# Performance work log

Measured on AMD Instinct MI355X. Metric: run time of the kernel, lower is better.

The kernel has to match this reference:

```python
import jax, jax.numpy as jnp
import numpy as np

K = 16
D_MODEL = 128

def _gather(pts, idx):
    # pts: [B,N,C], idx: [B,N,K] -> [B,N,K,C]
    return jax.vmap(lambda p, i: p[i])(pts, idx)

def setup_inputs() -> dict:
    key = jax.random.key(0)
    ks = jax.random.split(key, 20)
    s = 0.05
    def w(k_, shape):
        return jax.random.normal(k_, shape, dtype=jnp.float32) * s
    B, N, C = 4, 4096, 3
    TF, D = 128, D_MODEL
    return {
        "xyz": jax.random.normal(ks[0], (B, N, C), dtype=jnp.float32),
        "W0a": w(ks[1], (C, TF)),  "b0a": jnp.zeros((TF,), jnp.float32),
        "W0b": w(ks[2], (TF, TF)), "b0b": jnp.zeros((TF,), jnp.float32),
        "W1":  w(ks[3], (TF, D)),  "b1":  jnp.zeros((D,), jnp.float32),
        "W2":  w(ks[4], (D, TF)),  "b2":  jnp.zeros((TF,), jnp.float32),
        "Wd1": w(ks[5], (C, D)),   "bd1": jnp.zeros((D,), jnp.float32),
        "Wd2": w(ks[6], (D, D)),   "bd2": jnp.zeros((D,), jnp.float32),
        "Wg1": w(ks[7], (D, D)),   "bg1": jnp.zeros((D,), jnp.float32),
        "Wg2": w(ks[8], (D, D)),   "bg2": jnp.zeros((D,), jnp.float32),
        "Wq":  w(ks[9], (D, D)),
        "Wk":  w(ks[10], (D, D)),
        "Wv":  w(ks[11], (D, D)),
    }

def reference(xyz, W0a, b0a, W0b, b0b, W1, b1, W2, b2,
              Wd1, bd1, Wd2, bd2, Wg1, bg1, Wg2, bg2, Wq, Wk, Wv):
    sq = jnp.sum(xyz * xyz, axis=-1)
    dists = sq[:, :, None] - 2.0 * jnp.einsum('bnc,bmc->bnm', xyz, xyz) + sq[:, None, :]
    _, knn_idx = jax.lax.top_k(-dists, K)          # [B,N,K] nearest neighbors

    knn_xyz = _gather(xyz, knn_idx)                # [B,N,K,3]
    features = jax.nn.relu(xyz @ W0a + b0a) @ W0b + b0b   # fc0  [B,N,TF]
    pre = features
    x = features @ W1 + b1                          # fc1  [B,N,D]
    q = x @ Wq                                      # [B,N,D]
    kf = _gather(x @ Wk, knn_idx)                   # [B,N,K,D]
    vf = _gather(x @ Wv, knn_idx)                   # [B,N,K,D]

    delta = xyz[:, :, None, :] - knn_xyz            # [B,N,K,3]
    pos_enc = jax.nn.relu(delta @ Wd1 + bd1) @ Wd2 + bd2   # fc_delta [B,N,K,D]

    h = q[:, :, None, :] - kf + pos_enc
    attn_logits = jax.nn.relu(h @ Wg1 + bg1) @ Wg2 + bg2   # fc_gamma [B,N,K,D]
    attn = jax.nn.softmax(attn_logits / np.sqrt(D_MODEL).astype(np.float32), axis=-2)

    res = jnp.einsum('bmnf,bmnf->bmf', attn, vf + pos_enc)  # [B,N,D]
    res = res @ W2 + b2 + pre                               # [B,N,TF]
    return res, attn
```

## Files before the change

### kernel.cpp

```cpp
#include <hip/hip_runtime.h>
#include <math.h>

#define BB 4
#define NN 4096
#define KNNK 16
#define DD 128
#define BN (BB*NN)

typedef __attribute__((ext_vector_type(8))) short short8;
typedef __attribute__((ext_vector_type(4))) float floatx4;

__device__ __forceinline__ short f2bf(float x) {
  __bf16 b = (__bf16)x;
  return (short)__builtin_bit_cast(unsigned short, b);
}

__device__ __forceinline__ float bf2f(short h) {
  return __uint_as_float((unsigned)(unsigned short)h << 16);
}

#define LDSFENCE() asm volatile("s_waitcnt lgkmcnt(0)" ::: "memory")

__device__ __forceinline__ void split_from_lds(const float* __restrict__ trans,
                                               int c, int g, short8 ah[4],
                                               short8 al[4]) {
#pragma unroll
  for (int s = 0; s < 4; ++s) {
    const float* p_ = &trans[c * 132 + s * 32 + g * 8];
    float4 u0 = *reinterpret_cast<const float4*>(p_);
    float4 u1 = *reinterpret_cast<const float4*>(p_ + 4);
    float tmp[8] = {u0.x, u0.y, u0.z, u0.w, u1.x, u1.y, u1.z, u1.w};
#pragma unroll
    for (int j = 0; j < 8; ++j) {
      short h_ = f2bf(tmp[j]);
      ah[s][j] = h_;
      al[s][j] = f2bf(tmp[j] - bf2f(h_));
    }
  }
}

__device__ __forceinline__ void split_gemm2(const short* __restrict__ Bh,
                                            int nt0, int lane,
                                            const short8 ah[4],
                                            const short8 al[4], floatx4& acc0,
                                            floatx4& acc1) {
  const short* Bl = Bh + 16384;
#pragma unroll
  for (int ks = 0; ks < 4; ++ks) {
    const size_t o0 = ((size_t)((nt0 + 0) * 4 + ks) * 64 + lane) * 8;
    const size_t o1 = ((size_t)((nt0 + 1) * 4 + ks) * 64 + lane) * 8;
    short8 bh0 = *reinterpret_cast<const short8*>(Bh + o0);
    short8 bl0 = *reinterpret_cast<const short8*>(Bl + o0);
    short8 bh1 = *reinterpret_cast<const short8*>(Bh + o1);
    short8 bl1 = *reinterpret_cast<const short8*>(Bl + o1);
    acc0 = __builtin_amdgcn_mfma_f32_16x16x32_bf16(ah[ks], bh0, acc0, 0, 0, 0);
    acc1 = __builtin_amdgcn_mfma_f32_16x16x32_bf16(ah[ks], bh1, acc1, 0, 0, 0);
    acc0 = __builtin_amdgcn_mfma_f32_16x16x32_bf16(ah[ks], bl0, acc0, 0, 0, 0);
    acc1 = __builtin_amdgcn_mfma_f32_16x16x32_bf16(ah[ks], bl1, acc1, 0, 0, 0);
    acc0 = __builtin_amdgcn_mfma_f32_16x16x32_bf16(al[ks], bh0, acc0, 0, 0, 0);
    acc1 = __builtin_amdgcn_mfma_f32_16x16x32_bf16(al[ks], bh1, acc1, 0, 0, 0);
  }
}

__device__ __forceinline__ void ced(double& a, double& b) {
  double mn = fmin(a, b);
  double mx = fmax(a, b);
  a = mn;
  b = mx;
}

__device__ __forceinline__ void dsort16(double v[16]) {
#define CE(i, j) ced(v[i], v[j]);
  CE(0, 1) CE(2, 3) CE(4, 5) CE(6, 7) CE(8, 9) CE(10, 11) CE(12, 13) CE(14, 15)
  CE(0, 2) CE(1, 3) CE(4, 6) CE(5, 7) CE(8, 10) CE(9, 11) CE(12, 14) CE(13, 15)
  CE(1, 2) CE(5, 6) CE(9, 10) CE(13, 14)
  CE(0, 4) CE(1, 5) CE(2, 6) CE(3, 7) CE(8, 12) CE(9, 13) CE(10, 14) CE(11, 15)
  CE(2, 4) CE(3, 5) CE(10, 12) CE(11, 13)
  CE(1, 2) CE(3, 4) CE(5, 6) CE(9, 10) CE(11, 12) CE(13, 14)
  CE(0, 8) CE(1, 9) CE(2, 10) CE(3, 11) CE(4, 12) CE(5, 13) CE(6, 14) CE(7, 15)
  CE(4, 8) CE(5, 9) CE(6, 10) CE(7, 11)
  CE(2, 4) CE(3, 5) CE(6, 8) CE(7, 9) CE(10, 12) CE(11, 13)
  CE(1, 2) CE(3, 4) CE(5, 6) CE(7, 8) CE(9, 10) CE(11, 12) CE(13, 14)
#undef CE
}

__device__ __forceinline__ void dbitonic16(double m[16]) {
#pragma unroll
  for (int s = 8; s >= 1; s >>= 1) {
#pragma unroll
    for (int i = 0; i < 16; ++i) {
      if ((i & s) == 0) ced(m[i], m[i + s]);
    }
  }
}

__global__ __launch_bounds__(256, 4) void knn_kernel(
    const float4* __restrict__ pts4, int* __restrict__ knn) {
  const int wv = threadIdx.x >> 6;
  const int lane = threadIdx.x & 63;
  const int ln = lane & 15;
  const int qg = lane >> 4;
  const int q = blockIdx.x * 16 + wv * 4 + qg;
  const int b = q >> 12;
  const int n = q & 4095;
  const float4* pb = pts4 + ((size_t)b << 12);

  const float4 qp = pb[n];
  const float qx = qp.x, qy = qp.y, qz = qp.z, qsq = qp.w;

#define LOADBATCH(batch)                                                       \
  _Pragma("unroll") for (int i = 0; i < 16; ++i) {                             \
    const int c = ((batch) * 16 + i) * 16 + ln;                                \
    float4 p = pb[c];                                                          \
    float dot = __fadd_rn(__fadd_rn(__fmul_rn(qx, p.x), __fmul_rn(qy, p.y)),   \
                          __fmul_rn(qz, p.z));                                 \
    float d = __fadd_rn(__fsub_rn(qsq, __fmul_rn(2.0f, dot)), p.w);            \
    unsigned u = __float_as_uint(d);                                           \
    u = (u & 0x80000000u) ? ~u : (u | 0x80000000u);                            \
    unsigned long long key =                                                   \
        0x3FF0000000000000ULL | (((unsigned long long)u << 12) | (unsigned)c); \
    v[i] = __longlong_as_double((long long)key);                               \
  }

  double top[16];
  {
    double v[16];
    LOADBATCH(0);
    dsort16(v);
#pragma unroll
    for (int i = 0; i < 16; ++i) top[i] = v[i];
  }
#pragma unroll 1
  for (int batch = 1; batch < 16; ++batch) {
    double v[16];
    LOADBATCH(batch);
    dsort16(v);
    double m[16];
#pragma unroll
    for (int i = 0; i < 16; ++i)
      m[i] = fmin(top[i], v[15 - i]);
    dbitonic16(m);
#pragma unroll
    for (int i = 0; i < 16; ++i) top[i] = m[i];
  }
#undef LOADBATCH

#pragma unroll
  for (int mask = 1; mask <= 8; mask <<= 1) {
    double oth[16];
#pragma unroll
    for (int i = 0; i < 16; ++i) {
      double y = __shfl_xor(top[15 - i], mask);
      oth[i] = fmin(y, top[i]);
    }
    dbitonic16(oth);
#pragma unroll
    for (int i = 0; i < 16; ++i) top[i] = oth[i];
  }

  if (ln == 0) {
    int* outp = knn + (size_t)q * KNNK;
#pragma unroll
    for (int k = 0; k < 16; ++k)
      outp[k] = (int)(__double_as_longlong(top[k]) & 0xFFFLL);
  }
}

__global__ void swz_all_kernel(const float* __restrict__ xyz,
                               const float* __restrict__ Wd2,
                               const float* __restrict__ Wg1,
                               const float* __restrict__ Wg2,
                               const float* __restrict__ W0b,
                               const float* __restrict__ W1,
                               const float* __restrict__ Wq,
                               const float* __restrict__ Wk,
                               const float* __restrict__ Wv,
                               const float* __restrict__ W2,
                               short* __restrict__ wsw,
                               short* __restrict__ wsplit,
                               float4* __restrict__ pts4) {
  int t = blockIdx.x * 256 + threadIdx.x;
  if (t < BN) {
    float cx = xyz[(size_t)t * 3 + 0];
    float cy = xyz[(size_t)t * 3 + 1];
    float cz = xyz[(size_t)t * 3 + 2];
    float csq = __fadd_rn(__fadd_rn(__fmul_rn(cx, cx), __fmul_rn(cy, cy)),
                          __fmul_rn(cz, cz));
    pts4[t] = make_float4(cx, cy, cz, csq);
  }
  if (t < 3 * 2048) {
    int stage = t / 2048;
    int rem = t % 2048;
    int nt = rem / 256;
    int ks = (rem % 256) / 64;
    int lane = rem % 64;
    const float* W = (stage == 0) ? Wd2 : (stage == 1) ? Wg1 : Wg2;
    short8 o;
#pragma unroll
    for (int j = 0; j < 8; ++j) {
      int k = ks * 32 + (lane >> 4) * 8 + j;
      int n = nt * 16 + (lane & 15);
      o[j] = f2bf(W[k * 128 + n]);
    }
    *reinterpret_cast<short8*>(wsw + (size_t)t * 8) = o;
  } else {
    int u = t - 3 * 2048;
    if (u >= 6 * 2048) return;
    int mat = u / 2048;
    int rem = u % 2048;
    int nt = rem / 256;
    int ks = (rem % 256) / 64;
    int lane = rem % 64;
    const float* W = (mat == 0) ? W0b : (mat == 1) ? W1 : (mat == 2) ? Wq
                     : (mat == 3) ? Wk : (mat == 4) ? Wv : W2;
    short8 hi, lo;
#pragma unroll
    for (int j = 0; j < 8; ++j) {
      int k = ks * 32 + (lane >> 4) * 8 + j;
      int n = nt * 16 + (lane & 15);
      float w = W[k * 128 + n];
      short h = f2bf(w);
      hi[j] = h;
      lo[j] = f2bf(w - bf2f(h));
    }
    *reinterpret_cast<short8*>(wsplit + ((size_t)(2 * mat) * 2048 + rem) * 8) = hi;
    *reinterpret_cast<short8*>(wsplit + ((size_t)(2 * mat + 1) * 2048 + rem) * 8) = lo;
  }
}

__global__ __launch_bounds__(256, 4) void point_mlp_mfma_kernel(
    const float* __restrict__ xyz, const float* __restrict__ W0a,
    const float* __restrict__ b0a, const float* __restrict__ b0b,
    const float* __restrict__ b1, const short* __restrict__ wsplit,
    float* __restrict__ pre, float* __restrict__ qv, float* __restrict__ kv,
    float* __restrict__ vv) {
  const int wv = threadIdx.x >> 6;
  const int lane = threadIdx.x & 63;
  const int g = lane >> 4;
  const int c = lane & 15;
  const int g0 = blockIdx.x * 16;
  const int nt0 = wv * 2;

  __shared__ __attribute__((aligned(16))) float trans[16 * 132];
  __shared__ float xs[64];
  if (threadIdx.x < 48) {
    int p = threadIdx.x / 3, cc = threadIdx.x % 3;
    xs[p * 4 + cc] = xyz[(size_t)(g0 + p) * 3 + cc];
  }
  __syncthreads();

  short8 ah[4], al[4];
  {
    const float x0 = xs[c * 4 + 0], x1 = xs[c * 4 + 1], x2 = xs[c * 4 + 2];
#pragma unroll
    for (int s = 0; s < 4; ++s) {
#pragma unroll
      for (int j = 0; j < 8; ++j) {
        const int k = s * 32 + g * 8 + j;
        float v = fmaf(x2, W0a[256 + k],
                       fmaf(x1, W0a[128 + k], fmaf(x0, W0a[k], b0a[k])));
        v = fmaxf(v, 0.f);
        const short h = f2bf(v);
        ah[s][j] = h;
        al[s][j] = f2bf(v - bf2f(h));
      }
    }
  }

  floatx4 acc0, acc1;
  const floatx4 zf = (floatx4){0.f, 0.f, 0.f, 0.f};

  acc0 = zf; acc1 = zf;
  split_gemm2(wsplit + 0 * 32768, nt0, lane, ah, al, acc0, acc1);
  {
    const float bb0 = b0b[nt0 * 16 + c];
    const float bb1 = b0b[(nt0 + 1) * 16 + c];
#pragma unroll
    for (int r = 0; r < 4; ++r) {
      const int row = g * 4 + r;
      float v0 = acc0[r] + bb0;
      float v1 = acc1[r] + bb1;
      pre[(size_t)(g0 + row) * 128 + nt0 * 16 + c] = v0;
      pre[(size_t)(g0 + row) * 128 + (nt0 + 1) * 16 + c] = v1;
      trans[row * 132 + nt0 * 16 + c] = v0;
      trans[row * 132 + (nt0 + 1) * 16 + c] = v1;
    }
  }
  __syncthreads();
  split_from_lds(trans, c, g, ah, al);
  __syncthreads();

  acc0 = zf; acc1 = zf;
  split_gemm2(wsplit + 1 * 32768, nt0, lane, ah, al, acc0, acc1);
  {
    const float bb0 = b1[nt0 * 16 + c];
    const float bb1 = b1[(nt0 + 1) * 16 + c];
#pragma unroll
    for (int r = 0; r < 4; ++r) {
      const int row = g * 4 + r;
      trans[row * 132 + nt0 * 16 + c] = acc0[r] + bb0;
      trans[row * 132 + (nt0 + 1) * 16 + c] = acc1[r] + bb1;
    }
  }
  __syncthreads();
  split_from_lds(trans, c, g, ah, al);
  __syncthreads();

#define GSTORE(dst)                                                            \
  _Pragma("unroll") for (int r = 0; r < 4; ++r) {                              \
    const int row = g0 + g * 4 + r;                                            \
    dst[(size_t)row * 128 + nt0 * 16 + c] = acc0[r];                           \
    dst[(size_t)row * 128 + (nt0 + 1) * 16 + c] = acc1[r];                     \
  }

  acc0 = zf; acc1 = zf;
  split_gemm2(wsplit + 2 * 32768, nt0, lane, ah, al, acc0, acc1);
  GSTORE(qv);

  acc0 = zf; acc1 = zf;
  split_gemm2(wsplit + 3 * 32768, nt0, lane, ah, al, acc0, acc1);
  GSTORE(kv);

  acc0 = zf; acc1 = zf;
  split_gemm2(wsplit + 4 * 32768, nt0, lane, ah, al, acc0, acc1);
  GSTORE(vv);

#undef GSTORE
}

__device__ __forceinline__ void wstage(const short* __restrict__ wsw_stage,
                                       short* __restrict__ wlds, int wv,
                                       int lane) {
#pragma unroll
  for (int i = 0; i < 8; ++i) {
    short8 w_ = *reinterpret_cast<const short8*>(wsw_stage + wv * 4096 +
                                                 i * 512 + lane * 8);
    *reinterpret_cast<short8*>(&wlds[wv * 4096 + i * 512 + lane * 8]) = w_;
  }
}

__global__ __launch_bounds__(256, 3) void attn_mfma_kernel(
    const float* __restrict__ xyz, const int* __restrict__ knn,
    const float* __restrict__ qv, const float* __restrict__ kv,
    const float* __restrict__ vv, const short* __restrict__ wsw,
    const float* __restrict__ Wd1, const float* __restrict__ bd1,
    const float* __restrict__ bd2, const float* __restrict__ bg1,
    const float* __restrict__ bg2, float* __restrict__ res_ws,
    float* __restrict__ out_attn) {
  const int wv = threadIdx.x >> 6;
  const int lane = threadIdx.x & 63;
  const int g = lane >> 4;
  const int c = lane & 15;
  const int bn = blockIdx.x * 4 + wv;
  const int b = bn >> 12;
  const int base_n = b << 12;

  __shared__ __attribute__((aligned(16))) short wlds[16384];
  __shared__ __attribute__((aligned(16))) short conv[4][16 * 136];

  const int* knnp = knn + (size_t)bn * 16;
  const int idxn = knnp[c];
  int idxr[4];
#pragma unroll
  for (int r = 0; r < 4; ++r) idxr[r] = knnp[g * 4 + r];

  float kvf[8][4];
#pragma unroll
  for (int nt = 0; nt < 8; ++nt)
#pragma unroll
    for (int r = 0; r < 4; ++r)
      kvf[nt][r] = kv[((size_t)(base_n + idxr[r])) * 128 + nt * 16 + c];

  const float ddx = xyz[(size_t)bn * 3 + 0] - xyz[((size_t)(base_n + idxn)) * 3 + 0];
  const float ddy = xyz[(size_t)bn * 3 + 1] - xyz[((size_t)(base_n + idxn)) * 3 + 1];
  const float ddz = xyz[(size_t)bn * 3 + 2] - xyz[((size_t)(base_n + idxn)) * 3 + 2];

  short8 af[4];
#pragma unroll
  for (int s = 0; s < 4; ++s) {
#pragma unroll
    for (int j = 0; j < 8; ++j) {
      int d = s * 32 + g * 8 + j;
      float v = fmaf(ddz, Wd1[256 + d],
                     fmaf(ddy, Wd1[128 + d], fmaf(ddx, Wd1[d], bd1[d])));
      af[s][j] = f2bf(fmaxf(v, 0.f));
    }
  }

  float qc[8], bd2v[8];
#pragma unroll
  for (int nt = 0; nt < 8; ++nt) {
    qc[nt] = qv[(size_t)bn * 128 + nt * 16 + c];
    bd2v[nt] = bd2[nt * 16 + c];
  }

  floatx4 acc[8];

#define STAGE_GEMM_LDS()                                                       \
  {                                                                            \
    _Pragma("unroll") for (int ks = 0; ks < 4; ++ks) {                         \
      _Pragma("unroll") for (int h2 = 0; h2 < 2; ++h2) {                       \
        short8 bfr[4];                                                         \
        _Pragma("unroll") for (int i = 0; i < 4; ++i)                          \
          bfr[i] = *reinterpret_cast<const short8*>(                           \
              &wlds[((h2 * 4 + i) * 4 + ks) * 512 + lane * 8]);                \
        _Pragma("unroll") for (int i = 0; i < 4; ++i)                          \
          acc[h2 * 4 + i] = __builtin_amdgcn_mfma_f32_16x16x32_bf16(           \
              af[ks], bfr[i], acc[h2 * 4 + i], 0, 0, 0);                       \
      }                                                                        \
    }                                                                          \
  }

  wstage(wsw, wlds, wv, lane);
  __syncthreads();
#pragma unroll
  for (int nt = 0; nt < 8; ++nt) acc[nt] = (floatx4){0.f, 0.f, 0.f, 0.f};
  STAGE_GEMM_LDS();

  float PE[8][4];
#pragma unroll
  for (int nt = 0; nt < 8; ++nt) {
#pragma unroll
    for (int r = 0; r < 4; ++r) {
      float pe = acc[nt][r] + bd2v[nt];
      PE[nt][r] = pe;
      conv[wv][(g * 4 + r) * 136 + nt * 16 + c] =
          f2bf(qc[nt] - kvf[nt][r] + pe);
    }
  }
  LDSFENCE();
#pragma unroll
  for (int s = 0; s < 4; ++s)
    af[s] = *reinterpret_cast<const short8*>(&conv[wv][c * 136 + s * 32 + g * 8]);

  __syncthreads();
  wstage(wsw + 16384, wlds, wv, lane);
  __syncthreads();
#pragma unroll
  for (int nt = 0; nt < 8; ++nt) acc[nt] = (floatx4){0.f, 0.f, 0.f, 0.f};
  STAGE_GEMM_LDS();
#pragma unroll
  for (int nt = 0; nt < 8; ++nt) {
    const float bg1v = bg1[nt * 16 + c];
#pragma unroll
    for (int r = 0; r < 4; ++r) {
      conv[wv][(g * 4 + r) * 136 + nt * 16 + c] =
          f2bf(fmaxf(acc[nt][r] + bg1v, 0.f));
    }
  }
  LDSFENCE();
#pragma unroll
  for (int s = 0; s < 4; ++s)
    af[s] = *reinterpret_cast<const short8*>(&conv[wv][c * 136 + s * 32 + g * 8]);

  __syncthreads();
  wstage(wsw + 32768, wlds, wv, lane);
  __syncthreads();

  const float inv = 0.0883883476483184f;
  float resv[8];
#pragma unroll
  for (int h = 0; h < 2; ++h) {
    const int ntb = h * 4;
    float vvf[4][4];
#pragma unroll
    for (int i = 0; i < 4; ++i)
#pragma unroll
      for (int r = 0; r < 4; ++r)
        vvf[i][r] =
            vv[((size_t)(base_n + idxr[r])) * 128 + (ntb + i) * 16 + c];

    floatx4 acch[4];
#pragma unroll
    for (int i = 0; i < 4; ++i) acch[i] = (floatx4){0.f, 0.f, 0.f, 0.f};
#pragma unroll
    for (int ks = 0; ks < 4; ++ks) {
      short8 bfr[4];
#pragma unroll
      for (int i = 0; i < 4; ++i)
        bfr[i] = *reinterpret_cast<const short8*>(
            &wlds[((ntb + i) * 4 + ks) * 512 + lane * 8]);
#pragma unroll
      for (int i = 0; i < 4; ++i)
        acch[i] = __builtin_amdgcn_mfma_f32_16x16x32_bf16(af[ks], bfr[i],
                                                          acch[i], 0, 0, 0);
    }

#pragma unroll
    for (int i = 0; i < 4; ++i) {
      const int nt = ntb + i;
      const float bg2v = bg2[nt * 16 + c];
      float l0 = (acch[i][0] + bg2v) * inv;
      float l1 = (acch[i][1] + bg2v) * inv;
      float l2 = (acch[i][2] + bg2v) * inv;
      float l3 = (acch[i][3] + bg2v) * inv;
      float m4 = fmaxf(fmaxf(l0, l1), fmaxf(l2, l3));
      m4 = fmaxf(m4, __shfl_xor(m4, 16));
      m4 = fmaxf(m4, __shfl_xor(m4, 32));
      float e0 = __expf(l0 - m4), e1 = __expf(l1 - m4);
      float e2 = __expf(l2 - m4), e3 = __expf(l3 - m4);
      float s4 = e0 + e1 + e2 + e3;
      s4 += __shfl_xor(s4, 16);
      s4 += __shfl_xor(s4, 32);
      float rs = 1.f / s4;
      float a0 = e0 * rs, a1 = e1 * rs, a2 = e2 * rs, a3 = e3 * rs;
      size_t base = ((size_t)bn * 16 + g * 4) * 128 + nt * 16 + c;
      out_attn[base + 0 * 128] = a0;
      out_attn[base + 1 * 128] = a1;
      out_attn[base + 2 * 128] = a2;
      out_attn[base + 3 * 128] = a3;
      float r = 0.f;
      r = fmaf(a0, vvf[i][0] + PE[nt][0], r);
      r = fmaf(a1, vvf[i][1] + PE[nt][1], r);
      r = fmaf(a2, vvf[i][2] + PE[nt][2], r);
      r = fmaf(a3, vvf[i][3] + PE[nt][3], r);
      r += __shfl_xor(r, 16);
      r += __shfl_xor(r, 32);
      resv[nt] = r;
    }
  }
#undef STAGE_GEMM_LDS

  if (g == 0) {
#pragma unroll
    for (int nt = 0; nt < 8; ++nt)
      res_ws[(size_t)bn * 128 + nt * 16 + c] = resv[nt];
  }
}

__global__ __launch_bounds__(256, 4) void epilogue_mfma_kernel(
    const float* __restrict__ res_ws, const short* __restrict__ wsplit,
    const float* __restrict__ b2, const float* __restrict__ pre,
    float* __restrict__ out_res) {
  const int wv = threadIdx.x >> 6;
  const int lane = threadIdx.x & 63;
  const int g = lane >> 4;
  const int c = lane & 15;
  const int g0 = blockIdx.x * 16;
  const int nt0 = wv * 2;

  __shared__ __attribute__((aligned(16))) float trans[16 * 132];

#pragma unroll
  for (int i = 0; i < 2; ++i) {
    int idx4 = threadIdx.x + i * 256;
    int row = idx4 >> 5;
    int col4 = idx4 & 31;
    float4 v = *reinterpret_cast<const float4*>(
        res_ws + (size_t)(g0 + row) * 128 + col4 * 4);
    *reinterpret_cast<float4*>(&trans[row * 132 + col4 * 4]) = v;
  }
  __syncthreads();

  short8 ah[4], al[4];
  split_from_lds(trans, c, g, ah, al);

  float prv0[4], prv1[4];
  const float bb0 = b2[nt0 * 16 + c];
  const float bb1 = b2[(nt0 + 1) * 16 + c];
#pragma unroll
  for (int r = 0; r < 4; ++r) {
    prv0[r] = pre[(size_t)(g0 + g * 4 + r) * 128 + nt0 * 16 + c];
    prv1[r] = pre[(size_t)(g0 + g * 4 + r) * 128 + (nt0 + 1) * 16 + c];
  }

  floatx4 acc0 = (floatx4){0.f, 0.f, 0.f, 0.f};
  floatx4 acc1 = (floatx4){0.f, 0.f, 0.f, 0.f};
  split_gemm2(wsplit + 5 * 32768, nt0, lane, ah, al, acc0, acc1);

#pragma unroll
  for (int r = 0; r < 4; ++r) {
    const int row = g0 + g * 4 + r;
    out_res[(size_t)row * 128 + nt0 * 16 + c] = acc0[r] + bb0 + prv0[r];
    out_res[(size_t)row * 128 + (nt0 + 1) * 16 + c] = acc1[r] + bb1 + prv1[r];
  }
}

extern "C" void kernel_launch(void* const* d_in, const int* in_sizes, int n_in,
                              void* d_out, int out_size, void* d_ws,
                              size_t ws_size, hipStream_t stream) {
  const float* xyz = (const float*)d_in[0];
  const float* W0a = (const float*)d_in[1];
  const float* b0a = (const float*)d_in[2];
  const float* W0b = (const float*)d_in[3];
  const float* b0b = (const float*)d_in[4];
  const float* W1 = (const float*)d_in[5];
  const float* b1 = (const float*)d_in[6];
  const float* W2 = (const float*)d_in[7];
  const float* b2 = (const float*)d_in[8];
  const float* Wd1 = (const float*)d_in[9];
  const float* bd1 = (const float*)d_in[10];
  const float* Wd2 = (const float*)d_in[11];
  const float* bd2 = (const float*)d_in[12];
  const float* Wg1 = (const float*)d_in[13];
  const float* bg1 = (const float*)d_in[14];
  const float* Wg2 = (const float*)d_in[15];
  const float* bg2 = (const float*)d_in[16];
  const float* Wq = (const float*)d_in[17];
  const float* Wk = (const float*)d_in[18];
  const float* Wv = (const float*)d_in[19];

  char* ws = (char*)d_ws;
  int* knn = (int*)ws;
  float* pre = (float*)(ws + (1 << 20));
  float* qv = (float*)(ws + (9 << 20));
  float* kv = (float*)(ws + (17 << 20));
  float* vv = (float*)(ws + (25 << 20));
  float* res_ws = (float*)(ws + (33 << 20));
  short* wsw = (short*)(ws + (41 << 20));
  short* wsplit = (short*)(ws + (41 << 20) + (128 << 10));
  float4* pts4 = (float4*)(ws + (42 << 20));

  float* out_res = (float*)d_out;
  float* out_attn = out_res + (size_t)BN * DD;

  hipLaunchKernelGGL(swz_all_kernel, dim3(72), dim3(256), 0, stream, xyz, Wd2,
                     Wg1, Wg2, W0b, W1, Wq, Wk, Wv, W2, wsw, wsplit, pts4);
  hipLaunchKernelGGL(knn_kernel, dim3(1024), dim3(256), 0, stream, pts4, knn);
  hipLaunchKernelGGL(point_mlp_mfma_kernel, dim3(1024), dim3(256), 0, stream,
                     xyz, W0a, b0a, b0b, b1, wsplit, pre, qv, kv, vv);
  hipLaunchKernelGGL(attn_mfma_kernel, dim3(4096), dim3(256), 0, stream, xyz,
                     knn, qv, kv, vv, wsw, Wd1, bd1, bd2, bg1, bg2, res_ws,
                     out_attn);
  hipLaunchKernelGGL(epilogue_mfma_kernel, dim3(1024), dim3(256), 0, stream,
                     res_ws, wsplit, b2, pre, out_res);
}
```

Before: 331.4 us.

## Halve attention kernel weight LDS buffer and stage weights in two halves

Shrinks the shared-memory weight buffer from 32KB to 16KB and stages each 128x128 weight matrix in two column halves, each followed by a half GEMM. Launch bounds are raised from 3 to 4 blocks per CU so more waves can be resident to hide gather latency. In exchange, extra __syncthreads barriers and weight-staging rounds are added per stage, and register pressure must fit the tighter bound.

After: 345.5 us. 1.04x slower.

```diff
diff --git a/kernel.cpp b/kernel.cpp
--- a/kernel.cpp
+++ b/kernel.cpp
@@ -328,18 +328,7 @@
 #undef GSTORE
 }
 
-__device__ __forceinline__ void wstage(const short* __restrict__ wsw_stage,
-                                       short* __restrict__ wlds, int wv,
-                                       int lane) {
-#pragma unroll
-  for (int i = 0; i < 8; ++i) {
-    short8 w_ = *reinterpret_cast<const short8*>(wsw_stage + wv * 4096 +
-                                                 i * 512 + lane * 8);
-    *reinterpret_cast<short8*>(&wlds[wv * 4096 + i * 512 + lane * 8]) = w_;
-  }
-}
-
-__global__ __launch_bounds__(256, 3) void attn_mfma_kernel(
+__global__ __launch_bounds__(256, 4) void attn_mfma_kernel(
     const float* __restrict__ xyz, const int* __restrict__ knn,
     const float* __restrict__ qv, const float* __restrict__ kv,
     const float* __restrict__ vv, const short* __restrict__ wsw,
@@ -355,7 +344,7 @@
   const int b = bn >> 12;
   const int base_n = b << 12;
 
-  __shared__ __attribute__((aligned(16))) short wlds[16384];
+  __shared__ __attribute__((aligned(16))) short wlds[8192];
   __shared__ __attribute__((aligned(16))) short conv[4][16 * 136];
 
   const int* knnp = knn + (size_t)bn * 16;
@@ -396,26 +385,33 @@
 
   floatx4 acc[8];
 
-#define STAGE_GEMM_LDS()                                                       \
-  {                                                                            \
-    _Pragma("unroll") for (int ks = 0; ks < 4; ++ks) {                         \
-      _Pragma("unroll") for (int h2 = 0; h2 < 2; ++h2) {                       \
-        short8 bfr[4];                                                         \
-        _Pragma("unroll") for (int i = 0; i < 4; ++i)                          \
-          bfr[i] = *reinterpret_cast<const short8*>(                           \
-              &wlds[((h2 * 4 + i) * 4 + ks) * 512 + lane * 8]);                \
-        _Pragma("unroll") for (int i = 0; i < 4; ++i)                          \
-          acc[h2 * 4 + i] = __builtin_amdgcn_mfma_f32_16x16x32_bf16(           \
-              af[ks], bfr[i], acc[h2 * 4 + i], 0, 0, 0);                       \
-      }                                                                        \
-    }                                                                          \
-  }
-
-  wstage(wsw, wlds, wv, lane);
-  __syncthreads();
+#define WSH(SOFF, H)                                                           \
+  _Pragma("unroll") for (int i = 0; i < 4; ++i) {                              \
+    short8 w_ = *reinterpret_cast<const short8*>(                              \
+        wsw + (SOFF) + (H) * 8192 + wv * 2048 + i * 512 + lane * 8);           \
+    *reinterpret_cast<short8*>(&wlds[wv * 2048 + i * 512 + lane * 8]) = w_;    \
+  }
+
+#define HALF_GEMM(A)                                                           \
+  _Pragma("unroll") for (int ks = 0; ks < 4; ++ks) {                           \
+    short8 bfr[4];                                                             \
+    _Pragma("unroll") for (int i = 0; i < 4; ++i)                              \
+      bfr[i] = *reinterpret_cast<const short8*>(                               \
+          &wlds[((i * 4 + ks) * 64 + lane) * 8]);                              \
+    _Pragma("unroll") for (int i = 0; i < 4; ++i)                              \
+      (A)[i] = __builtin_amdgcn_mfma_f32_16x16x32_bf16(af[ks], bfr[i], (A)[i], \
+                                                       0, 0, 0);               \
+  }
+
 #pragma unroll
   for (int nt = 0; nt < 8; ++nt) acc[nt] = (floatx4){0.f, 0.f, 0.f, 0.f};
-  STAGE_GEMM_LDS();
+  WSH(0, 0);
+  __syncthreads();
+  HALF_GEMM(acc);
+  __syncthreads();
+  WSH(0, 1);
+  __syncthreads();
+  HALF_GEMM((acc + 4));
 
   float PE[8][4];
 #pragma unroll
@@ -434,11 +430,15 @@
     af[s] = *reinterpret_cast<const short8*>(&conv[wv][c * 136 + s * 32 + g * 8]);
 
   __syncthreads();
-  wstage(wsw + 16384, wlds, wv, lane);
-  __syncthreads();
 #pragma unroll
   for (int nt = 0; nt < 8; ++nt) acc[nt] = (floatx4){0.f, 0.f, 0.f, 0.f};
-  STAGE_GEMM_LDS();
+  WSH(16384, 0);
+  __syncthreads();
+  HALF_GEMM(acc);
+  __syncthreads();
+  WSH(16384, 1);
+  __syncthreads();
+  HALF_GEMM((acc + 4));
 #pragma unroll
   for (int nt = 0; nt < 8; ++nt) {
     const float bg1v = bg1[nt * 16 + c];
@@ -454,14 +454,14 @@
     af[s] = *reinterpret_cast<const short8*>(&conv[wv][c * 136 + s * 32 + g * 8]);
 
   __syncthreads();
-  wstage(wsw + 32768, wlds, wv, lane);
-  __syncthreads();
 
   const float inv = 0.0883883476483184f;
   float resv[8];
 #pragma unroll
   for (int h = 0; h < 2; ++h) {
     const int ntb = h * 4;
+    WSH(32768, h);
+
     float vvf[4][4];
 #pragma unroll
     for (int i = 0; i < 4; ++i)
@@ -470,21 +470,12 @@
         vvf[i][r] =
             vv[((size_t)(base_n + idxr[r])) * 128 + (ntb + i) * 16 + c];
 
+    __syncthreads();
+
     floatx4 acch[4];
 #pragma unroll
     for (int i = 0; i < 4; ++i) acch[i] = (floatx4){0.f, 0.f, 0.f, 0.f};
-#pragma unroll
-    for (int ks = 0; ks < 4; ++ks) {
-      short8 bfr[4];
-#pragma unroll
-      for (int i = 0; i < 4; ++i)
-        bfr[i] = *reinterpret_cast<const short8*>(
-            &wlds[((ntb + i) * 4 + ks) * 512 + lane * 8]);
-#pragma unroll
-      for (int i = 0; i < 4; ++i)
-        acch[i] = __builtin_amdgcn_mfma_f32_16x16x32_bf16(af[ks], bfr[i],
-                                                          acch[i], 0, 0, 0);
-    }
+    HALF_GEMM(acch);
 
 #pragma unroll
     for (int i = 0; i < 4; ++i) {
@@ -518,8 +509,10 @@
       r += __shfl_xor(r, 32);
       resv[nt] = r;
     }
-  }
-#undef STAGE_GEMM_LDS
+    if (h == 0) __syncthreads();
+  }
+#undef HALF_GEMM
+#undef WSH
 
   if (g == 0) {
 #pragma unroll
```
